# Performance work log

Measured on AMD Instinct MI355X. Metric: run time of the kernel, lower is better.

Reference implementation:

```python
import jax, jax.numpy as jnp
import numpy as np

DECAY = 0.1   # self.decay
EPS = 1e-5    # self.eps
NORM_EPS = 1e-8


def setup_inputs() -> dict:
    key = jax.random.key(0)
    k1, k2, k3 = jax.random.split(key, 3)
    N, D, K, H = 65536, 32, 4096, 1
    x = jax.random.normal(k1, (N, D), dtype=jnp.float32)
    embed = jax.random.normal(k2, (H, K, D), dtype=jnp.float32)
    cluster_size = jnp.zeros((H, K), dtype=jnp.float32)
    embed_avg = jax.random.normal(k3, (H, K, D), dtype=jnp.float32)
    return {"x": x, "embed": embed, "cluster_size": cluster_size, "embed_avg": embed_avg}


def reference(x, embed, cluster_size, embed_avg):
    H, K, D = embed.shape
    orig_shape = x.shape
    # needs_codebook_dim: x.ndim < 4 -> add codebook dim, flatten to [h, n, d]
    f = x.reshape(H, -1, D).astype(jnp.float32)
    # L2-normalize features and codebook (as in forward)
    fn = f / (jnp.linalg.norm(f, axis=-1, keepdims=True) + NORM_EPS)
    en = embed / (jnp.linalg.norm(embed, axis=-1, keepdims=True) + NORM_EPS)
    # negative pairwise squared euclidean distance: [h, n, K]
    f2 = jnp.sum(fn * fn, axis=-1)[..., None]          # [h, n, 1]
    e2 = jnp.sum(en * en, axis=-1)[:, None, :]          # [h, 1, K]
    dist = -(f2 - 2.0 * jnp.einsum('hnd,hkd->hnk', fn, en) + e2)
    # hard assignment (argmax of negative distance == nearest code)
    embed_ind = jnp.argmax(dist, axis=-1)               # [h, n] int
    onehot = jax.nn.one_hot(embed_ind, K, dtype=fn.dtype)  # [h, n, K]
    # batched_embedding: one-hot @ codebook
    quantize = jnp.einsum('hnk,hkd->hnd', onehot, en)
    # EMA codebook statistics (batched_bincount + scatter-add of features)
    bins = jnp.sum(onehot, axis=1)                       # [h, K]
    embed_sum = jnp.einsum('hnd,hnk->hkd', fn, onehot)   # [h, K, d]
    cluster_size_new = cluster_size * DECAY + bins * (1.0 - DECAY)
    embed_avg_new = embed_avg * DECAY + embed_sum * (1.0 - DECAY)
    # laplace-smoothed normalization of the EMA codebook
    n_total = jnp.sum(cluster_size_new, axis=-1, keepdims=True)
    smoothed = (cluster_size_new + EPS) / (n_total + K * EPS) * n_total
    embed_updated = embed_avg_new / smoothed[..., None]
    quantize = quantize.reshape(orig_shape)
    return quantize, embed_ind, cluster_size_new, embed_avg_new, embed_updated
```

## Files before the change

kernel.cpp:

```cpp
#include <hip/hip_runtime.h>
#include <float.h>

#define DECAY 0.1f
#define OMD   0.9f
#define EPS   1e-5f
#define NORM_EPS 1e-8f

static constexpr int D = 32;

typedef __attribute__((ext_vector_type(8))) short s16x8;
typedef __attribute__((ext_vector_type(4))) float f32x4_t;

__device__ __forceinline__ float bf2f(short s) {
    return __uint_as_float(((unsigned int)(unsigned short)s) << 16);
}

struct Split3 { short b0, b1, b2; };

__device__ __forceinline__ Split3 split3(float v) {
    const unsigned int u0 = __float_as_uint(v) & 0xFFFF0000u;
    const float r  = v - __uint_as_float(u0);
    const unsigned int u1 = __float_as_uint(r) & 0xFFFF0000u;
    const float r2 = r - __uint_as_float(u1);
    Split3 s;
    s.b0 = (short)(u0 >> 16);
    s.b1 = (short)(u1 >> 16);
    s.b2 = (short)(__float_as_uint(r2) >> 16);
    return s;
}

__global__ void prep_codebook(const float* __restrict__ embed,
                              unsigned short* __restrict__ bfrag,
                              int K) {
    const int k = blockIdx.x * blockDim.x + threadIdx.x;
    if (k >= K) return;
    float v[D]; float ssq = 0.f;
#pragma unroll
    for (int d = 0; d < D; ++d) { v[d] = embed[(size_t)k * D + d]; ssq += v[d] * v[d]; }
    const float inv = 1.0f / (sqrtf(ssq) + NORM_EPS);
    float e2 = 0.f;
    short p0[D], p1[D], p2[D];
#pragma unroll
    for (int d = 0; d < D; ++d) {
        const float e = v[d] * inv;
        e2 += e * e;
        const Split3 s = split3(2.0f * e);
        p0[d] = s.b0; p1[d] = s.b1; p2[d] = s.b2;
    }
    char* base = (char*)bfrag + (size_t)(k >> 4) * 3136;
    const int col = k & 15;
    *(float*)(base + 3072 + col * 4) = -e2;
#pragma unroll
    for (int g = 0; g < 4; ++g) {
        const int lid = g * 16 + col;
        s16x8 s0, s1, s2;
#pragma unroll
        for (int i = 0; i < 8; ++i) { s0[i] = p0[g*8+i]; s1[i] = p1[g*8+i]; s2[i] = p2[g*8+i]; }
        *(s16x8*)(base +    0 + lid * 16) = s0;
        *(s16x8*)(base + 1024 + lid * 16) = s1;
        *(s16x8*)(base + 2048 + lid * 16) = s2;
    }
}

struct Btile { s16x8 b0, b1, b2; float ne2; };

__global__ __launch_bounds__(512)
void assign_kernel(const float* __restrict__ x,
                   const unsigned short* __restrict__ bfrag,
                   float* __restrict__ out_quant,
                   float* __restrict__ out_ind,
                   float* __restrict__ bins,
                   float* __restrict__ esum,
                   int N, int K) {
    constexpr int PB = 32;
    __shared__ char  sm[6144];
    __shared__ float teamS[8][PB];
    __shared__ float teamC[8][PB];
    __shared__ int   best_c[PB];

    const int tid  = threadIdx.x;
    const int lane = tid & 63;
    const int team = tid >> 6;
    const int n0   = blockIdx.x * PB;
    const int col  = lane & 15;

    float fn_r[8];
    if (tid < 4 * PB) {
        const int p = tid >> 2, q = tid & 3;
        const float* xp = &x[(size_t)(n0 + p) * D + q * 8];
        const float4 va = *(const float4*)(xp);
        const float4 vb = *(const float4*)(xp + 4);
        float ssq = va.x*va.x + va.y*va.y + va.z*va.z + va.w*va.w
                  + vb.x*vb.x + vb.y*vb.y + vb.z*vb.z + vb.w*vb.w;
        ssq += __shfl_xor(ssq, 1);
        ssq += __shfl_xor(ssq, 2);
        const float inv = 1.0f / (sqrtf(ssq) + NORM_EPS);
        fn_r[0]=va.x*inv; fn_r[1]=va.y*inv; fn_r[2]=va.z*inv; fn_r[3]=va.w*inv;
        fn_r[4]=vb.x*inv; fn_r[5]=vb.y*inv; fn_r[6]=vb.z*inv; fn_r[7]=vb.w*inv;
        char* dst = &sm[(p >> 4) * 3072 + (q * 16 + (p & 15)) * 16];
        s16x8 s0, s1, s2;
#pragma unroll
        for (int i = 0; i < 8; ++i) {
            const Split3 s = split3(fn_r[i]);
            s0[i] = s.b0; s1[i] = s.b1; s2[i] = s.b2;
        }
        *(s16x8*)(dst) = s0; *(s16x8*)(dst + 1024) = s1; *(s16x8*)(dst + 2048) = s2;
    }
    __syncthreads();

    s16x8 A[2][3];
#pragma unroll
    for (int pg = 0; pg < 2; ++pg) {
#pragma unroll
        for (int pl = 0; pl < 3; ++pl)
            A[pg][pl] = *(const s16x8*)&sm[pg * 3072 + pl * 1024 + lane * 16];
    }

    float bestS[2][4], bestC[2][4];
#pragma unroll
    for (int pg = 0; pg < 2; ++pg)
#pragma unroll
        for (int r = 0; r < 4; ++r) { bestS[pg][r] = -1e30f; bestC[pg][r] = 0.f; }

    const int NT = K >> 4;
    const int HT = NT >> 3;
    const int t0 = team * HT;
    const char* gp  = (const char*)bfrag + (size_t)t0 * 3136 + lane * 16;
    const char* gpe = (const char*)bfrag + (size_t)t0 * 3136 + 3072 + (size_t)col * 4;

    auto compute = [&](const Btile& T, float codef) {
        const f32x4_t initX = {T.ne2, T.ne2, T.ne2, T.ne2};
#pragma unroll
        for (int pg = 0; pg < 2; ++pg) {
            f32x4_t X = __builtin_amdgcn_mfma_f32_16x16x32_bf16(A[pg][0], T.b0, initX, 0, 0, 0);
            X = __builtin_amdgcn_mfma_f32_16x16x32_bf16(A[pg][0], T.b1, X, 0, 0, 0);
            X = __builtin_amdgcn_mfma_f32_16x16x32_bf16(A[pg][1], T.b1, X, 0, 0, 0);
            X = __builtin_amdgcn_mfma_f32_16x16x32_bf16(A[pg][1], T.b0, X, 0, 0, 0);
            X = __builtin_amdgcn_mfma_f32_16x16x32_bf16(A[pg][0], T.b2, X, 0, 0, 0);
            X = __builtin_amdgcn_mfma_f32_16x16x32_bf16(A[pg][2], T.b0, X, 0, 0, 0);
#pragma unroll
            for (int r = 0; r < 4; ++r) {
                const float sc = X[r];
                if (sc > bestS[pg][r]) { bestS[pg][r] = sc; bestC[pg][r] = codef; }
            }
        }
    };

    auto loadB = [&](const char* base, const char* ebase, Btile& T) {
        T.b0  = *(const s16x8*)(base);
        T.b1  = *(const s16x8*)(base + 1024);
        T.b2  = *(const s16x8*)(base + 2048);
        T.ne2 = *(const float*)(ebase);
    };

    Btile U, V;
    loadB(gp,        gpe,        U);
    loadB(gp + 3136, gpe + 3136, V);

    float cb = (float)(t0 * 16 + col);
    for (int t = 0; t < HT; t += 2) {
        compute(U, cb);
        loadB(gp + 2 * 3136, gpe + 2 * 3136, U);
        compute(V, cb + 16.0f);
        loadB(gp + 3 * 3136, gpe + 3 * 3136, V);
        gp += 6272; gpe += 6272;
        cb += 32.0f;
    }

#pragma unroll
    for (int pg = 0; pg < 2; ++pg)
#pragma unroll
        for (int r = 0; r < 4; ++r) {
            float s = bestS[pg][r], c = bestC[pg][r];
#pragma unroll
            for (int off = 8; off >= 1; off >>= 1) {
                const float os = __shfl_xor(s, off);
                const float oc = __shfl_xor(c, off);
                if (os > s || (os == s && oc < c)) { s = os; c = oc; }
            }
            if (col == 0) {
                const int p = pg * 16 + (lane >> 4) * 4 + r;
                teamS[team][p] = s;
                teamC[team][p] = c;
            }
        }
    __syncthreads();

    if (tid < PB) {
        float s = teamS[0][tid];
        float c = teamC[0][tid];
#pragma unroll
        for (int t = 1; t < 8; ++t) {
            const float st = teamS[t][tid];
            const float ct = teamC[t][tid];
            if (st > s) { s = st; c = ct; }
        }
        out_ind[n0 + tid] = c;
        best_c[tid] = (int)c;
        atomicAdd(&bins[(int)c], 1.0f);
    }
    __syncthreads();

    if (tid < 4 * PB) {
        const int p = tid >> 2, q = tid & 3;
        const int b = best_c[p];
#pragma unroll
        for (int i = 0; i < 8; ++i)
            atomicAdd(&esum[(size_t)b * D + q * 8 + i], fn_r[i]);
        const char* bp = (const char*)bfrag + (size_t)(b >> 4) * 3136;
        const int lid = q * 16 + (b & 15);
        const s16x8 s0 = *(const s16x8*)(bp +    0 + lid * 16);
        const s16x8 s1 = *(const s16x8*)(bp + 1024 + lid * 16);
        const s16x8 s2 = *(const s16x8*)(bp + 2048 + lid * 16);
        float o[8];
#pragma unroll
        for (int i = 0; i < 8; ++i)
            o[i] = 0.5f * ((bf2f(s0[i]) + bf2f(s1[i])) + bf2f(s2[i]));
        float4 q0 = {o[0], o[1], o[2], o[3]};
        float4 q1 = {o[4], o[5], o[6], o[7]};
        *(float4*)&out_quant[(size_t)(n0 + p) * D + q * 8]     = q0;
        *(float4*)&out_quant[(size_t)(n0 + p) * D + q * 8 + 4] = q1;
    }
}

__global__ void reduce_kernel(const float* __restrict__ cluster_size,
                              const float* __restrict__ bins,
                              float* __restrict__ out_cs,
                              float* __restrict__ n_total, int K) {
    __shared__ float red[256];
    float s = 0.f;
    for (int k = threadIdx.x; k < K; k += 256) {
        const float v = cluster_size[k] * DECAY + bins[k] * OMD;
        out_cs[k] = v;
        s += v;
    }
    red[threadIdx.x] = s;
    __syncthreads();
    for (int off = 128; off > 0; off >>= 1) {
        if (threadIdx.x < off) red[threadIdx.x] += red[threadIdx.x + off];
        __syncthreads();
    }
    if (threadIdx.x == 0) n_total[0] = red[0];
}

__global__ void finalize_kernel(const float* __restrict__ embed_avg,
                                const float* __restrict__ esum,
                                const float* __restrict__ out_cs,
                                const float* __restrict__ n_total,
                                float* __restrict__ out_avg,
                                float* __restrict__ out_upd,
                                int K) {
    const int i = blockIdx.x * blockDim.x + threadIdx.x;
    if (i >= K * D) return;
    const int k = i >> 5;
    const float avg = embed_avg[i] * DECAY + esum[i] * OMD;
    out_avg[i] = avg;
    const float nt = n_total[0];
    const float cs = out_cs[k];
    const float sm = (cs + EPS) / (nt + (float)K * EPS) * nt;
    out_upd[i] = avg / sm;
}

extern "C" void kernel_launch(void* const* d_in, const int* in_sizes, int n_in,
                              void* d_out, int out_size, void* d_ws, size_t ws_size,
                              hipStream_t stream) {
    const float* x            = (const float*)d_in[0];
    const float* embed        = (const float*)d_in[1];
    const float* cluster_size = (const float*)d_in[2];
    const float* embed_avg    = (const float*)d_in[3];

    const int KD = in_sizes[1];
    const int K  = in_sizes[2];
    const int N  = in_sizes[0] / D;

    float* ws = (float*)d_ws;
    unsigned short* bfrag = (unsigned short*)ws;
    float* bins  = ws + (size_t)K * 49;
    float* esum  = bins + K;
    float* ntot  = esum + KD;

    float* out     = (float*)d_out;
    float* o_quant = out;
    float* o_ind   = o_quant + (size_t)N * D;
    float* o_cs    = o_ind   + N;
    float* o_avg   = o_cs    + K;
    float* o_upd   = o_avg   + KD;

    (void)hipMemsetAsync(bins, 0, (size_t)(K + KD + 1) * sizeof(float), stream);

    prep_codebook<<<(K + 63) / 64, 64, 0, stream>>>(embed, bfrag, K);
    assign_kernel<<<N / 32, 512, 0, stream>>>(x, bfrag,
                                              o_quant, o_ind, bins, esum, N, K);
    reduce_kernel<<<1, 256, 0, stream>>>(cluster_size, bins, o_cs, ntot, K);
    finalize_kernel<<<(KD + 255) / 256, 256, 0, stream>>>(embed_avg, esum, o_cs, ntot,
                                                          o_avg, o_upd, K);
}
```

Before: 133.8 us.

## Split codebook across blocks with 64-bit atomicMax argmax and separate scatter kernel

Reorganizes the assignment so each block handles 256 points against one eighth of the codebook, with each wave holding its own 32 points. Partial argmaxes are merged through a packed 64-bit atomicMax on global memory, which replaces the in-block team reduction. The scatter of quantize, bins and embed_sum moves into a separate kernel that recomputes the normalization and accumulates directly into the output average, which is pre-seeded by a new kernel. The aim is to cut codebook reloads per point and raise per-block work. The cost is extra launches, an N×8-byte packed buffer with its memset, and more global atomics.

```diff
diff --git a/kernel.cpp b/kernel.cpp
--- a/kernel.cpp
+++ b/kernel.cpp
@@ -62,49 +62,61 @@
     }
 }
 
+__global__ void seed_avg(const float* __restrict__ embed_avg,
+                         float* __restrict__ o_avg, int KD) {
+    const int i = blockIdx.x * 256 + threadIdx.x;
+    if (i < KD) o_avg[i] = embed_avg[i] * DECAY;
+}
+
 struct Btile { s16x8 b0, b1, b2; float ne2; };
 
 __global__ __launch_bounds__(512)
 void assign_kernel(const float* __restrict__ x,
                    const unsigned short* __restrict__ bfrag,
-                   float* __restrict__ out_quant,
-                   float* __restrict__ out_ind,
-                   float* __restrict__ bins,
-                   float* __restrict__ esum,
+                   unsigned long long* __restrict__ packed,
                    int N, int K) {
-    constexpr int PB = 32;
-    __shared__ char  sm[6144];
-    __shared__ float teamS[8][PB];
-    __shared__ float teamC[8][PB];
-    __shared__ int   best_c[PB];
+    __shared__ char sm[49152];
 
     const int tid  = threadIdx.x;
     const int lane = tid & 63;
-    const int team = tid >> 6;
-    const int n0   = blockIdx.x * PB;
+    const int w    = tid >> 6;
+    const int bid  = blockIdx.x;
+    const int team = bid & 7;
+    const int n0   = (bid >> 3) * 256;
     const int col  = lane & 15;
-
-    float fn_r[8];
-    if (tid < 4 * PB) {
-        const int p = tid >> 2, q = tid & 3;
-        const float* xp = &x[(size_t)(n0 + p) * D + q * 8];
+    char* wbase = &sm[w * 6144];
+
+    {
+        const int pw = lane >> 1, h = lane & 1;
+        const float* xp = &x[(size_t)(n0 + w * 32 + pw) * D + h * 16];
         const float4 va = *(const float4*)(xp);
         const float4 vb = *(const float4*)(xp + 4);
+        const float4 vc = *(const float4*)(xp + 8);
+        const float4 vd = *(const float4*)(xp + 12);
         float ssq = va.x*va.x + va.y*va.y + va.z*va.z + va.w*va.w
-                  + vb.x*vb.x + vb.y*vb.y + vb.z*vb.z + vb.w*vb.w;
+                  + vb.x*vb.x + vb.y*vb.y + vb.z*vb.z + vb.w*vb.w
+                  + vc.x*vc.x + vc.y*vc.y + vc.z*vc.z + vc.w*vc.w
+                  + vd.x*vd.x + vd.y*vd.y + vd.z*vd.z + vd.w*vd.w;
         ssq += __shfl_xor(ssq, 1);
-        ssq += __shfl_xor(ssq, 2);
         const float inv = 1.0f / (sqrtf(ssq) + NORM_EPS);
-        fn_r[0]=va.x*inv; fn_r[1]=va.y*inv; fn_r[2]=va.z*inv; fn_r[3]=va.w*inv;
-        fn_r[4]=vb.x*inv; fn_r[5]=vb.y*inv; fn_r[6]=vb.z*inv; fn_r[7]=vb.w*inv;
-        char* dst = &sm[(p >> 4) * 3072 + (q * 16 + (p & 15)) * 16];
-        s16x8 s0, s1, s2;
-#pragma unroll
-        for (int i = 0; i < 8; ++i) {
-            const Split3 s = split3(fn_r[i]);
-            s0[i] = s.b0; s1[i] = s.b1; s2[i] = s.b2;
+        float fr[16];
+        fr[0]=va.x*inv;  fr[1]=va.y*inv;  fr[2]=va.z*inv;  fr[3]=va.w*inv;
+        fr[4]=vb.x*inv;  fr[5]=vb.y*inv;  fr[6]=vb.z*inv;  fr[7]=vb.w*inv;
+        fr[8]=vc.x*inv;  fr[9]=vc.y*inv;  fr[10]=vc.z*inv; fr[11]=vc.w*inv;
+        fr[12]=vd.x*inv; fr[13]=vd.y*inv; fr[14]=vd.z*inv; fr[15]=vd.w*inv;
+        const int pg = pw >> 4;
+#pragma unroll
+        for (int cc = 0; cc < 2; ++cc) {
+            const int q = 2 * h + cc;
+            char* dst = wbase + pg * 3072 + (q * 16 + (pw & 15)) * 16;
+            s16x8 s0, s1, s2;
+#pragma unroll
+            for (int i = 0; i < 8; ++i) {
+                const Split3 s = split3(fr[cc * 8 + i]);
+                s0[i] = s.b0; s1[i] = s.b1; s2[i] = s.b2;
+            }
+            *(s16x8*)(dst) = s0; *(s16x8*)(dst + 1024) = s1; *(s16x8*)(dst + 2048) = s2;
         }
-        *(s16x8*)(dst) = s0; *(s16x8*)(dst + 1024) = s1; *(s16x8*)(dst + 2048) = s2;
     }
     __syncthreads();
 
@@ -113,7 +125,7 @@
     for (int pg = 0; pg < 2; ++pg) {
 #pragma unroll
         for (int pl = 0; pl < 3; ++pl)
-            A[pg][pl] = *(const s16x8*)&sm[pg * 3072 + pl * 1024 + lane * 16];
+            A[pg][pl] = *(const s16x8*)(wbase + pg * 3072 + pl * 1024 + lane * 16);
     }
 
     float bestS[2][4], bestC[2][4];
@@ -165,6 +177,7 @@
         loadB(gp + 3 * 3136, gpe + 3 * 3136, V);
         gp += 6272; gpe += 6272;
         cb += 32.0f;
+        if ((t & 7) == 6) __syncthreads();
     }
 
 #pragma unroll
@@ -180,47 +193,63 @@
             }
             if (col == 0) {
                 const int p = pg * 16 + (lane >> 4) * 4 + r;
-                teamS[team][p] = s;
-                teamC[team][p] = c;
+                const int gpt = n0 + w * 32 + p;
+                const unsigned int su = __float_as_uint(s);
+                const unsigned int ord = (su >> 31) ? ~su : (su | 0x80000000u);
+                const unsigned long long pk =
+                    ((unsigned long long)ord << 32) | (unsigned int)(~(unsigned int)(int)c);
+                atomicMax(&packed[gpt], pk);
             }
         }
-    __syncthreads();
-
-    if (tid < PB) {
-        float s = teamS[0][tid];
-        float c = teamC[0][tid];
-#pragma unroll
-        for (int t = 1; t < 8; ++t) {
-            const float st = teamS[t][tid];
-            const float ct = teamC[t][tid];
-            if (st > s) { s = st; c = ct; }
-        }
-        out_ind[n0 + tid] = c;
-        best_c[tid] = (int)c;
-        atomicAdd(&bins[(int)c], 1.0f);
-    }
-    __syncthreads();
-
-    if (tid < 4 * PB) {
-        const int p = tid >> 2, q = tid & 3;
-        const int b = best_c[p];
-#pragma unroll
-        for (int i = 0; i < 8; ++i)
-            atomicAdd(&esum[(size_t)b * D + q * 8 + i], fn_r[i]);
-        const char* bp = (const char*)bfrag + (size_t)(b >> 4) * 3136;
-        const int lid = q * 16 + (b & 15);
-        const s16x8 s0 = *(const s16x8*)(bp +    0 + lid * 16);
-        const s16x8 s1 = *(const s16x8*)(bp + 1024 + lid * 16);
-        const s16x8 s2 = *(const s16x8*)(bp + 2048 + lid * 16);
-        float o[8];
-#pragma unroll
-        for (int i = 0; i < 8; ++i)
-            o[i] = 0.5f * ((bf2f(s0[i]) + bf2f(s1[i])) + bf2f(s2[i]));
-        float4 q0 = {o[0], o[1], o[2], o[3]};
-        float4 q1 = {o[4], o[5], o[6], o[7]};
-        *(float4*)&out_quant[(size_t)(n0 + p) * D + q * 8]     = q0;
-        *(float4*)&out_quant[(size_t)(n0 + p) * D + q * 8 + 4] = q1;
-    }
+}
+
+__global__ __launch_bounds__(256)
+void scatter_kernel(const float* __restrict__ x,
+                    const unsigned short* __restrict__ bfrag,
+                    const unsigned long long* __restrict__ packed,
+                    float* __restrict__ out_quant,
+                    float* __restrict__ out_ind,
+                    float* __restrict__ bins,
+                    float* __restrict__ o_avg,
+                    int N) {
+    const int gid = blockIdx.x * 256 + threadIdx.x;
+    const int p = gid >> 2, q = gid & 3;
+    if (p >= N) return;
+    const float* xp = &x[(size_t)p * D + q * 8];
+    const float4 va = *(const float4*)(xp);
+    const float4 vb = *(const float4*)(xp + 4);
+    float ssq = va.x*va.x + va.y*va.y + va.z*va.z + va.w*va.w
+              + vb.x*vb.x + vb.y*vb.y + vb.z*vb.z + vb.w*vb.w;
+    ssq += __shfl_xor(ssq, 1);
+    ssq += __shfl_xor(ssq, 2);
+    const float inv = 1.0f / (sqrtf(ssq) + NORM_EPS);
+    float fn[8];
+    fn[0]=va.x*inv; fn[1]=va.y*inv; fn[2]=va.z*inv; fn[3]=va.w*inv;
+    fn[4]=vb.x*inv; fn[5]=vb.y*inv; fn[6]=vb.z*inv; fn[7]=vb.w*inv;
+
+    const unsigned long long pk = packed[p];
+    const int b = (int)(~(unsigned int)(pk & 0xFFFFFFFFull));
+    if (q == 0) {
+        out_ind[p] = (float)b;
+        atomicAdd(&bins[b], 1.0f);
+    }
+#pragma unroll
+    for (int i = 0; i < 8; ++i)
+        atomicAdd(&o_avg[(size_t)b * D + q * 8 + i], fn[i] * OMD);
+
+    const char* bp = (const char*)bfrag + (size_t)(b >> 4) * 3136;
+    const int lid = q * 16 + (b & 15);
+    const s16x8 s0 = *(const s16x8*)(bp +    0 + lid * 16);
+    const s16x8 s1 = *(const s16x8*)(bp + 1024 + lid * 16);
+    const s16x8 s2 = *(const s16x8*)(bp + 2048 + lid * 16);
+    float o[8];
+#pragma unroll
+    for (int i = 0; i < 8; ++i)
+        o[i] = 0.5f * ((bf2f(s0[i]) + bf2f(s1[i])) + bf2f(s2[i]));
+    float4 q0 = {o[0], o[1], o[2], o[3]};
+    float4 q1 = {o[4], o[5], o[6], o[7]};
+    *(float4*)&out_quant[(size_t)p * D + q * 8]     = q0;
+    *(float4*)&out_quant[(size_t)p * D + q * 8 + 4] = q1;
 }
 
 __global__ void reduce_kernel(const float* __restrict__ cluster_size,
@@ -243,22 +272,17 @@
     if (threadIdx.x == 0) n_total[0] = red[0];
 }
 
-__global__ void finalize_kernel(const float* __restrict__ embed_avg,
-                                const float* __restrict__ esum,
-                                const float* __restrict__ out_cs,
-                                const float* __restrict__ n_total,
-                                float* __restrict__ out_avg,
-                                float* __restrict__ out_upd,
-                                int K) {
+__global__ void upd_kernel(const float* __restrict__ o_avg,
+                           const float* __restrict__ out_cs,
+                           const float* __restrict__ n_total,
+                           float* __restrict__ o_upd, int K) {
     const int i = blockIdx.x * blockDim.x + threadIdx.x;
     if (i >= K * D) return;
     const int k = i >> 5;
-    const float avg = embed_avg[i] * DECAY + esum[i] * OMD;
-    out_avg[i] = avg;
     const float nt = n_total[0];
     const float cs = out_cs[k];
     const float sm = (cs + EPS) / (nt + (float)K * EPS) * nt;
-    out_upd[i] = avg / sm;
+    o_upd[i] = o_avg[i] / sm;
 }
 
 extern "C" void kernel_launch(void* const* d_in, const int* in_sizes, int n_in,
@@ -275,9 +299,9 @@
 
     float* ws = (float*)d_ws;
     unsigned short* bfrag = (unsigned short*)ws;
-    float* bins  = ws + (size_t)K * 49;
-    float* esum  = bins + K;
-    float* ntot  = esum + KD;
+    unsigned long long* packed = (unsigned long long*)(ws + (size_t)K * 49);
+    float* bins = (float*)((char*)packed + (size_t)N * 8);
+    float* ntot = bins + K;
 
     float* out     = (float*)d_out;
     float* o_quant = out;
@@ -286,12 +310,13 @@
     float* o_avg   = o_cs    + K;
     float* o_upd   = o_avg   + KD;
 
-    (void)hipMemsetAsync(bins, 0, (size_t)(K + KD + 1) * sizeof(float), stream);
+    (void)hipMemsetAsync(packed, 0, (size_t)N * 8 + ((size_t)K + 1) * sizeof(float), stream);
 
     prep_codebook<<<(K + 63) / 64, 64, 0, stream>>>(embed, bfrag, K);
-    assign_kernel<<<N / 32, 512, 0, stream>>>(x, bfrag,
-                                              o_quant, o_ind, bins, esum, N, K);
+    seed_avg<<<(KD + 255) / 256, 256, 0, stream>>>(embed_avg, o_avg, KD);
+    assign_kernel<<<(N / 256) * 8, 512, 0, stream>>>(x, bfrag, packed, N, K);
+    scatter_kernel<<<(N * 4) / 256, 256, 0, stream>>>(x, bfrag, packed,
+                                                      o_quant, o_ind, bins, o_avg, N);
     reduce_kernel<<<1, 256, 0, stream>>>(cluster_size, bins, o_cs, ntot, K);
-    finalize_kernel<<<(KD + 255) / 256, 256, 0, stream>>>(embed_avg, esum, o_cs, ntot,
-                                                          o_avg, o_upd, K);
-}
+    upd_kernel<<<(KD + 255) / 256, 256, 0, stream>>>(o_avg, o_cs, ntot, o_upd, K);
+}
```

New measurement: 180.8 us. +35.1%, slower.
